# Performance work log

Hardware: AMD Instinct MI355X
Metric: run time of the kernel (lower is better)

## Reference

```python
import jax, jax.numpy as jnp
import numpy as np

D = 256        # n_unit
H = 2          # n_head
FF = 256       # n_hid
WIN = 99       # N-1 in source: row i attends to cols [i-99, i]
NEG = -1e30    # additive mask value (-inf in torch)
LN_EPS = 1e-5


def _layer_norm(x, w, b):
    mu = jnp.mean(x, axis=-1, keepdims=True)
    var = jnp.mean((x - mu) ** 2, axis=-1, keepdims=True)
    return (x - mu) * jax.lax.rsqrt(var + LN_EPS) * w + b


def _pos_encoding(S, d):
    pos = jnp.arange(S, dtype=jnp.float32)[:, None]                      # [S,1]
    div = jnp.exp(jnp.arange(0, d, 2, dtype=jnp.float32) * (-np.log(10000.0) / d))
    ang = pos * div                                                      # [S,d/2]
    return jnp.stack([jnp.sin(ang), jnp.cos(ang)], axis=-1).reshape(S, d)


def _band_mask(S):
    i = jnp.arange(S)[:, None]
    j = jnp.arange(S)[None, :]
    allowed = (j <= i) & (j >= i - WIN)
    return jnp.where(allowed, 0.0, NEG).astype(jnp.float32)             # [S,S]


def setup_inputs() -> dict:
    key = jax.random.key(0)
    ks = jax.random.split(key, 24)
    B, S, IN = 8, 2000, 256
    s = 0.02
    inp = {
        "src": jax.random.normal(ks[0], (B, S, IN), jnp.float32),
        "input_lengths": jax.random.randint(ks[1], (B,), 1, S + 1).astype(jnp.int64),
        # encoder Linear(in_size, n_unit); torch Linear weight is [out,in]
        "W_enc": jax.random.normal(ks[2], (D, IN), jnp.float32) * s,
        "b_enc": jnp.zeros((D,), jnp.float32),
        # MHA packed qkv projection
        "in_proj_w": jax.random.normal(ks[3], (3 * D, D), jnp.float32) * s,
        "in_proj_b": jnp.zeros((3 * D,), jnp.float32),
        "out_proj_w": jax.random.normal(ks[4], (D, D), jnp.float32) * s,
        "out_proj_b": jnp.zeros((D,), jnp.float32),
        "ln1_w": jnp.ones((D,), jnp.float32),
        "ln1_b": jnp.zeros((D,), jnp.float32),
        # FFN
        "lin1_w": jax.random.normal(ks[5], (FF, D), jnp.float32) * s,
        "lin1_b": jnp.zeros((FF,), jnp.float32),
        "lin2_w": jax.random.normal(ks[6], (D, FF), jnp.float32) * s,
        "lin2_b": jnp.zeros((D,), jnp.float32),
        "ln2_w": jnp.ones((D,), jnp.float32),
        "ln2_b": jnp.zeros((D,), jnp.float32),
        # output head
        "fc1_w": jax.random.normal(ks[7], (D // 4, D), jnp.float32) * s,
        "fc1_b": jnp.zeros((D // 4,), jnp.float32),
        "fc2_w": jax.random.normal(ks[8], (1, D // 4), jnp.float32) * s,
        "fc2_b": jnp.zeros((1,), jnp.float32),
    }
    return inp


def reference(src, input_lengths, W_enc, b_enc, in_proj_w, in_proj_b,
              out_proj_w, out_proj_b, ln1_w, ln1_b, lin1_w, lin1_b,
              lin2_w, lin2_b, ln2_w, ln2_b, fc1_w, fc1_b, fc2_w, fc2_b):
    B, S, _ = src.shape
    hd = D // H
    # input projection + positional encoding (dropout is identity at eval)
    x = src @ W_enc.T + b_enc                                            # [B,S,D]
    x = x + _pos_encoding(S, D)[None]
    # --- TransformerEncoderLayer (post-norm, relu) with banded causal mask ---
    qkv = x @ in_proj_w.T + in_proj_b                                    # [B,S,3D]
    q, k, v = jnp.split(qkv, 3, axis=-1)
    q = q.reshape(B, S, H, hd)
    k = k.reshape(B, S, H, hd)
    v = v.reshape(B, S, H, hd)
    scores = jnp.einsum('bihd,bjhd->bhij', q, k) / np.sqrt(hd)           # [B,H,S,S]
    scores = scores + _band_mask(S)[None, None]
    attn = jax.nn.softmax(scores, axis=-1)
    ctx = jnp.einsum('bhij,bjhd->bihd', attn, v).reshape(B, S, D)
    attn_out = ctx @ out_proj_w.T + out_proj_b
    x = _layer_norm(x + attn_out, ln1_w, ln1_b)
    ff = jax.nn.relu(x @ lin1_w.T + lin1_b) @ lin2_w.T + lin2_b
    x = _layer_norm(x + ff, ln2_w, ln2_b)
    # --- output head (no activation between fc1 and fc2, per source) ---
    out = x @ fc1_w.T + fc1_b                                            # [B,S,D/4]
    logits = out @ fc2_w.T + fc2_b                                       # [B,S,1]
    return logits.reshape(B, -1)                                         # [B,S]
```

## Files before the change

kernel.cpp:

```cpp
#include <hip/hip_runtime.h>
#include <math.h>

#define SLEN 2000
#define BATCH 8
#define MTOK 16000
#define WIN 99
#define XPAD 264

typedef __attribute__((ext_vector_type(8))) short short8;
typedef __attribute__((ext_vector_type(4))) float floatx4;

#define WAITVM0() __builtin_amdgcn_s_waitcnt(0x0F70)
#define WAITVM4() __builtin_amdgcn_s_waitcnt(0x0F74)

__device__ __forceinline__ float bf2f(unsigned int h) {
  union { unsigned int u; float f; } w; w.u = h << 16; return w.f;
}
__device__ __forceinline__ unsigned short f2bf(float f) {
  union { float f; unsigned int u; } w; w.f = f;
  return (unsigned short)((w.u + 0x7fffu + ((w.u >> 16) & 1u)) >> 16);
}

typedef const __attribute__((address_space(1))) unsigned int* gas_t;
typedef __attribute__((address_space(3))) unsigned int* las_t;
__device__ __forceinline__ void gload_lds16(const unsigned short* g, unsigned short* l) {
  __builtin_amdgcn_global_load_lds((gas_t)g, (las_t)l, 16, 0, 0);
}

__device__ __forceinline__ void cvt4(const float* __restrict__ in,
                                     unsigned short* __restrict__ out, int i) {
  float4 v = ((const float4*)in)[i];
  ushort4 o;
  o.x = f2bf(v.x); o.y = f2bf(v.y); o.z = f2bf(v.z); o.w = f2bf(v.w);
  ((ushort4*)out)[i] = o;
}

__global__ __launch_bounds__(256) void k_prep(
    const float* __restrict__ wenc,     unsigned short* __restrict__ wencb,
    const float* __restrict__ wqk,      unsigned short* __restrict__ wqkb,
    const float* __restrict__ wout,     unsigned short* __restrict__ woutb,
    const float* __restrict__ wl1,      unsigned short* __restrict__ wl1b,
    const float* __restrict__ wl2,      unsigned short* __restrict__ wl2b,
    float* __restrict__ pe,
    const float* __restrict__ fc1w, const float* __restrict__ fc1b,
    const float* __restrict__ fc2w, const float* __restrict__ fc2b,
    const float* __restrict__ ln2w, const float* __restrict__ ln2b,
    float* __restrict__ hp) {
  __shared__ float red0[4], red1[4];
  const int bx = blockIdx.x, tid = threadIdx.x;
  if (bx < 64)         { cvt4(wenc, wencb, bx * 256 + tid); }
  else if (bx < 256)   { cvt4(wqk,  wqkb,  (bx - 64) * 256 + tid); }
  else if (bx < 320)   { cvt4(wout, woutb, (bx - 256) * 256 + tid); }
  else if (bx < 384)   { cvt4(wl1,  wl1b,  (bx - 320) * 256 + tid); }
  else if (bx < 448)   { cvt4(wl2,  wl2b,  (bx - 384) * 256 + tid); }
  else if (bx < 948) {
    int i4 = (bx - 448) * 256 + tid;
    int e0 = i4 * 4;
    int s  = e0 >> 8;
    int d0 = e0 & 255;
    float dv0 = expf((float)(d0 >> 1) * -0.07195578415606394f);
    float dv1 = expf((float)((d0 >> 1) + 1) * -0.07195578415606394f);
    float a0 = (float)s * dv0, a1 = (float)s * dv1;
    ((float4*)pe)[i4] = make_float4(sinf(a0), cosf(a0), sinf(a1), cosf(a1));
  } else {
    int k = tid;
    float we = 0.f;
#pragma unroll 8
    for (int o = 0; o < 64; ++o) we += fc2w[o] * fc1w[o * 256 + k];
    float c1 = ln2w[k] * we;
    hp[k] = c1;
    float p0 = ln2b[k] * we;
    if (k < 64) p0 += fc2w[k] * fc1b[k];
    float s0 = p0, s1 = c1;
#pragma unroll
    for (int off = 32; off; off >>= 1) {
      s0 += __shfl_xor(s0, off);
      s1 += __shfl_xor(s1, off);
    }
    int wv = k >> 6;
    if ((k & 63) == 0) { red0[wv] = s0; red1[wv] = s1; }
    __syncthreads();
    if (k == 0) {
      hp[256] = red0[0] + red0[1] + red0[2] + red0[3] + fc2b[0];
      hp[257] = red1[0] + red1[1] + red1[2] + red1[3];
    }
  }
}

__global__ __launch_bounds__(256) void k_pre(
    const float* __restrict__ src,
    const unsigned short* __restrict__ wenc, const float* __restrict__ benc,
    const float* __restrict__ pe,
    const unsigned short* __restrict__ wqk, const float* __restrict__ bqk,
    unsigned short* __restrict__ xb, unsigned short* __restrict__ qkvb) {
  __shared__ __align__(16) unsigned short Xt[64 * XPAD];
  __shared__ __align__(16) unsigned short Bst[4][2][2048];
  const int tid = threadIdx.x, lane = tid & 63, w = tid >> 6;
  const int m0 = blockIdx.x * 64;
  const int kq = lane >> 4, ml = lane & 15;
  const int wcolg = w * 64;

  int grow[4], gsc[4];
#pragma unroll
  for (int i = 0; i < 4; ++i) {
    grow[i] = i * 16 + (lane >> 2);
    gsc[i]  = (lane & 3) ^ ((grow[i] >> 1) & 3);
  }

  auto issueB = [&](const unsigned short* W, int kt, int buf) {
#pragma unroll
    for (int i = 0; i < 4; ++i)
      gload_lds16(W + (size_t)(wcolg + grow[i]) * 256 + kt + gsc[i] * 8,
                  &Bst[w][buf][i * 512]);
  };
  auto readB = [&](int buf, int nt) -> short8 {
    int n = nt * 16 + ml;
    int sb = kq ^ ((n >> 1) & 3);
    return *(const short8*)&Bst[w][buf][n * 32 + sb * 8];
  };

  floatx4 acc[4][4] = {};
#pragma unroll
  for (int k8 = 0; k8 < 8; ++k8) {
    const int kt = k8 * 32;
    issueB(wenc, kt, k8 & 1);
    short8 af[4];
#pragma unroll
    for (int mt = 0; mt < 4; ++mt) {
      const float* ap = src + (size_t)(m0 + mt * 16 + ml) * 256 + kt + kq * 8;
      float4 v0 = *(const float4*)ap;
      float4 v1 = *(const float4*)(ap + 4);
      unsigned short t8[8] = {f2bf(v0.x), f2bf(v0.y), f2bf(v0.z), f2bf(v0.w),
                              f2bf(v1.x), f2bf(v1.y), f2bf(v1.z), f2bf(v1.w)};
      af[mt] = *(const short8*)t8;
    }
    WAITVM0();
#pragma unroll
    for (int nt = 0; nt < 4; ++nt) {
      short8 bf = readB(k8 & 1, nt);
#pragma unroll
      for (int mt = 0; mt < 4; ++mt)
        acc[mt][nt] = __builtin_amdgcn_mfma_f32_16x16x32_bf16(af[mt], bf, acc[mt][nt], 0, 0, 0);
    }
  }
#pragma unroll
  for (int mt = 0; mt < 4; ++mt)
#pragma unroll
    for (int nt = 0; nt < 4; ++nt)
#pragma unroll
      for (int r = 0; r < 4; ++r) {
        int lrow = mt * 16 + kq * 4 + r;
        int col  = wcolg + nt * 16 + ml;
        float v = acc[mt][nt][r] + benc[col]
                + pe[(size_t)((m0 + lrow) % SLEN) * 256 + col];
        unsigned short hv = f2bf(v);
        Xt[lrow * XPAD + col] = hv;
        xb[(size_t)(m0 + lrow) * 256 + col] = hv;
      }
  __syncthreads();

  for (int p = 0; p < 3; ++p) {
    const unsigned short* Wp = wqk + (size_t)p * 65536;
    floatx4 a2[4][4] = {};
    issueB(Wp, 0, 0);
#pragma unroll
    for (int k8 = 0; k8 < 7; ++k8) {
      issueB(Wp, (k8 + 1) * 32, (k8 + 1) & 1);
      WAITVM4();
      short8 af[4];
#pragma unroll
      for (int mt = 0; mt < 4; ++mt)
        af[mt] = *(const short8*)&Xt[(mt * 16 + ml) * XPAD + k8 * 32 + kq * 8];
#pragma unroll
      for (int nt = 0; nt < 4; ++nt) {
        short8 bf = readB(k8 & 1, nt);
#pragma unroll
        for (int mt = 0; mt < 4; ++mt)
          a2[mt][nt] = __builtin_amdgcn_mfma_f32_16x16x32_bf16(af[mt], bf, a2[mt][nt], 0, 0, 0);
      }
    }
    WAITVM0();
    {
      short8 af[4];
#pragma unroll
      for (int mt = 0; mt < 4; ++mt)
        af[mt] = *(const short8*)&Xt[(mt * 16 + ml) * XPAD + 224 + kq * 8];
#pragma unroll
      for (int nt = 0; nt < 4; ++nt) {
        short8 bf = readB(1, nt);
#pragma unroll
        for (int mt = 0; mt < 4; ++mt)
          a2[mt][nt] = __builtin_amdgcn_mfma_f32_16x16x32_bf16(af[mt], bf, a2[mt][nt], 0, 0, 0);
      }
    }
#pragma unroll
    for (int mt = 0; mt < 4; ++mt)
#pragma unroll
      for (int nt = 0; nt < 4; ++nt)
#pragma unroll
        for (int r = 0; r < 4; ++r) {
          int row = m0 + mt * 16 + kq * 4 + r;
          int cg  = p * 256 + wcolg + nt * 16 + ml;
          qkvb[(size_t)row * 768 + cg] = f2bf(a2[mt][nt][r] + bqk[cg]);
        }
  }
}

#define KPAD 136
#define VPAD 184
#define PPAD 132
#define UNION 176

__global__ __launch_bounds__(256) void k_attn_mfma(const unsigned short* __restrict__ qkv,
                                                   unsigned short* __restrict__ ctx) {
  __shared__ __align__(16) unsigned short KV[UNION * KPAD];
  __shared__ __align__(16) unsigned short Ps[4][16 * PPAD];
  const int tid  = threadIdx.x;
  const int lane = tid & 63;
  const int w    = tid >> 6;
  const int i0   = blockIdx.x * 64;
  const int b    = blockIdx.y;
  const int h    = blockIdx.z;
  const int jmin_u = i0 - WIN;
  const float scale = 0.08838834764831845f;

  const int qrow = i0 + w * 16 + (lane & 15);
  const unsigned short* qptr =
      qkv + (size_t)(b * SLEN + min(qrow, SLEN - 1)) * 768 + h * 128 + (lane >> 4) * 8;
  short8 qf[4];
#pragma unroll
  for (int kc = 0; kc < 4; ++kc) qf[kc] = *(const short8*)(qptr + kc * 32);

  for (int it = 0; it < 11; ++it) {
    int idx = it * 256 + tid;
    int row = idx >> 4;
    int c8  = idx & 15;
    int j = jmin_u + row;
    uint4 v = make_uint4(0u, 0u, 0u, 0u);
    if (j >= 0 && j < SLEN)
      v = *(const uint4*)(qkv + (size_t)(b * SLEN + j) * 768 + 256 + h * 128 + c8 * 8);
    *(uint4*)&KV[row * KPAD + c8 * 8] = v;
  }
  __syncthreads();

  const int koff = w * 16;
  floatx4 sc[8] = {};
#pragma unroll
  for (int kt = 0; kt < 8; ++kt) {
#pragma unroll
    for (int kc = 0; kc < 4; ++kc) {
      short8 kf = *(const short8*)&KV[(koff + kt * 16 + (lane & 15)) * KPAD
                                      + kc * 32 + (lane >> 4) * 8];
      sc[kt] = __builtin_amdgcn_mfma_f32_16x16x32_bf16(qf[kc], kf, sc[kt], 0, 0, 0);
    }
  }

  const int qme = i0 + w * 16 + (lane >> 4) * 4;
  const int jme = jmin_u + koff + (lane & 15);
  float mx[4] = {-1e30f, -1e30f, -1e30f, -1e30f};
#pragma unroll
  for (int kt = 0; kt < 8; ++kt) {
#pragma unroll
    for (int r = 0; r < 4; ++r) {
      int j = jme + kt * 16, q = qme + r;
      bool ok = (j >= 0) && (j >= q - WIN) && (j <= q);
      float s = ok ? sc[kt][r] : -1e30f;
      sc[kt][r] = s;
      mx[r] = fmaxf(mx[r], s);
    }
  }
#pragma unroll
  for (int r = 0; r < 4; ++r)
#pragma unroll
    for (int off = 8; off; off >>= 1) mx[r] = fmaxf(mx[r], __shfl_xor(mx[r], off, 16));

  float sum[4] = {0.f, 0.f, 0.f, 0.f};
#pragma unroll
  for (int kt = 0; kt < 8; ++kt)
#pragma unroll
    for (int r = 0; r < 4; ++r) {
      float e = __expf((sc[kt][r] - mx[r]) * scale);
      sc[kt][r] = e;
      sum[r] += e;
    }
#pragma unroll
  for (int r = 0; r < 4; ++r)
#pragma unroll
    for (int off = 8; off; off >>= 1) sum[r] += __shfl_xor(sum[r], off, 16);
  float rinv[4];
#pragma unroll
  for (int r = 0; r < 4; ++r) rinv[r] = 1.f / sum[r];

  unsigned short* pw = &Ps[w][0];
#pragma unroll
  for (int kt = 0; kt < 8; ++kt)
#pragma unroll
    for (int r = 0; r < 4; ++r)
      pw[((lane >> 4) * 4 + r) * PPAD + kt * 16 + (lane & 15)] = f2bf(sc[kt][r]);
  __syncthreads();

  for (int it = 0; it < 12; ++it) {
    int idx = it * 256 + tid;
    int grp = idx >> 6;
    int key = (grp >> 4) * 64 + (idx & 63);
    int c8  = grp & 15;
    if (key < UNION) {
      int j = jmin_u + key;
      uint4 v = make_uint4(0u, 0u, 0u, 0u);
      if (j >= 0 && j < SLEN)
        v = *(const uint4*)(qkv + (size_t)(b * SLEN + j) * 768 + 512 + h * 128 + c8 * 8);
      unsigned short e[8];
      *(uint4*)e = v;
      int d0 = c8 * 8;
#pragma unroll
      for (int i = 0; i < 8; ++i) KV[(d0 + i) * VPAD + key] = e[i];
    }
  }
  __syncthreads();

  floatx4 ov[8] = {};
#pragma unroll
  for (int kc = 0; kc < 4; ++kc) {
    short8 pf = *(const short8*)&pw[(lane & 15) * PPAD + kc * 32 + (lane >> 4) * 8];
#pragma unroll
    for (int dt = 0; dt < 8; ++dt) {
      short8 vf = *(const short8*)&KV[(dt * 16 + (lane & 15)) * VPAD
                                      + koff + kc * 32 + (lane >> 4) * 8];
      ov[dt] = __builtin_amdgcn_mfma_f32_16x16x32_bf16(pf, vf, ov[dt], 0, 0, 0);
    }
  }

#pragma unroll
  for (int dt = 0; dt < 8; ++dt)
#pragma unroll
    for (int r = 0; r < 4; ++r) {
      int q = qme + r;
      if (q < SLEN)
        ctx[(size_t)(b * SLEN + q) * 256 + h * 128 + dt * 16 + (lane & 15)] =
            f2bf(ov[dt][r] * rinv[r]);
    }
}

__global__ __launch_bounds__(256) void k_post(
    const unsigned short* __restrict__ ctx,
    const unsigned short* __restrict__ wout, const float* __restrict__ bout,
    const unsigned short* __restrict__ xb,
    const float* __restrict__ ln1w, const float* __restrict__ ln1b,
    const unsigned short* __restrict__ w1, const float* __restrict__ b1,
    const unsigned short* __restrict__ w2, const float* __restrict__ b2,
    const float* __restrict__ hp, float* __restrict__ out) {
  __shared__ __align__(16) unsigned short X1[64 * XPAD];
  __shared__ __align__(16) unsigned short Bst[4][2][2048];
  __shared__ float lnred[4][64][3];
  __shared__ float lnstat[64][2];
  __shared__ float lnp[512];
  __shared__ float c1s[256];
  const int tid = threadIdx.x, lane = tid & 63, w = tid >> 6;
  const int m0 = blockIdx.x * 64;
  const int kq = lane >> 4, ml = lane & 15;
  const int wcolg = w * 64;

  lnp[tid] = ln1w[tid];
  lnp[256 + tid] = ln1b[tid];
  c1s[tid] = hp[tid];
  const float c0h = hp[256], sc1 = hp[257];

  int grow[4], gsc[4];
#pragma unroll
  for (int i = 0; i < 4; ++i) {
    grow[i] = i * 16 + (lane >> 2);
    gsc[i]  = (lane & 3) ^ ((grow[i] >> 1) & 3);
  }
  auto issueB = [&](const unsigned short* W, int kt, int buf) {
#pragma unroll
    for (int i = 0; i < 4; ++i)
      gload_lds16(W + (size_t)(wcolg + grow[i]) * 256 + kt + gsc[i] * 8,
                  &Bst[w][buf][i * 512]);
  };
  auto readB = [&](int buf, int nt) -> short8 {
    int n = nt * 16 + ml;
    int sb = kq ^ ((n >> 1) & 3);
    return *(const short8*)&Bst[w][buf][n * 32 + sb * 8];
  };

  floatx4 acc[4][4] = {};
#pragma unroll
  for (int k8 = 0; k8 < 8; ++k8) {
    const int kt = k8 * 32;
    issueB(wout, kt, k8 & 1);
    short8 af[4];
#pragma unroll
    for (int mt = 0; mt < 4; ++mt)
      af[mt] = *(const short8*)(ctx + (size_t)(m0 + mt * 16 + ml) * 256 + kt + kq * 8);
    WAITVM0();
#pragma unroll
    for (int nt = 0; nt < 4; ++nt) {
      short8 bf = readB(k8 & 1, nt);
#pragma unroll
      for (int mt = 0; mt < 4; ++mt)
        acc[mt][nt] = __builtin_amdgcn_mfma_f32_16x16x32_bf16(af[mt], bf, acc[mt][nt], 0, 0, 0);
    }
  }
  float s_[4][4], q_[4][4];
#pragma unroll
  for (int mt = 0; mt < 4; ++mt)
#pragma unroll
    for (int r = 0; r < 4; ++r) { s_[mt][r] = 0.f; q_[mt][r] = 0.f; }
#pragma unroll
  for (int mt = 0; mt < 4; ++mt)
#pragma unroll
    for (int nt = 0; nt < 4; ++nt)
#pragma unroll
      for (int r = 0; r < 4; ++r) {
        int lrow = mt * 16 + kq * 4 + r;
        int col  = wcolg + nt * 16 + ml;
        float v = acc[mt][nt][r] + bout[col]
                + bf2f(xb[(size_t)(m0 + lrow) * 256 + col]);
        acc[mt][nt][r] = v;
        s_[mt][r] += v;
        q_[mt][r] += v * v;
      }
#pragma unroll
  for (int mt = 0; mt < 4; ++mt)
#pragma unroll
    for (int r = 0; r < 4; ++r) {
#pragma unroll
      for (int off = 8; off; off >>= 1) {
        s_[mt][r] += __shfl_xor(s_[mt][r], off, 16);
        q_[mt][r] += __shfl_xor(q_[mt][r], off, 16);
      }
      if (ml == 0) {
        int lrow = mt * 16 + kq * 4 + r;
        lnred[w][lrow][0] = s_[mt][r];
        lnred[w][lrow][1] = q_[mt][r];
      }
    }
  __syncthreads();
  if (tid < 64) {
    float s = lnred[0][tid][0] + lnred[1][tid][0] + lnred[2][tid][0] + lnred[3][tid][0];
    float q = lnred[0][tid][1] + lnred[1][tid][1] + lnred[2][tid][1] + lnred[3][tid][1];
    float mu  = s * (1.f / 256.f);
    float var = q * (1.f / 256.f) - mu * mu;
    lnstat[tid][0] = mu;
    lnstat[tid][1] = rsqrtf(var + 1e-5f);
  }
  __syncthreads();
  floatx4 x1sav[4][4];
#pragma unroll
  for (int mt = 0; mt < 4; ++mt)
#pragma unroll
    for (int r = 0; r < 4; ++r) {
      int lrow = mt * 16 + kq * 4 + r;
      float mu = lnstat[lrow][0], rr = lnstat[lrow][1];
#pragma unroll
      for (int nt = 0; nt < 4; ++nt) {
        int col = wcolg + nt * 16 + ml;
        float x1 = (acc[mt][nt][r] - mu) * rr * lnp[col] + lnp[256 + col];
        x1sav[mt][nt][r] = x1;
        X1[lrow * XPAD + col] = f2bf(x1);
      }
    }
  __syncthreads();

#pragma unroll
  for (int mt = 0; mt < 4; ++mt)
#pragma unroll
    for (int nt = 0; nt < 4; ++nt) acc[mt][nt] = (floatx4){0.f, 0.f, 0.f, 0.f};
  issueB(w1, 0, 0);
#pragma unroll
  for (int k8 = 0; k8 < 7; ++k8) {
    issueB(w1, (k8 + 1) * 32, (k8 + 1) & 1);
    WAITVM4();
    short8 af[4];
#pragma unroll
    for (int mt = 0; mt < 4; ++mt)
      af[mt] = *(const short8*)&X1[(mt * 16 + ml) * XPAD + k8 * 32 + kq * 8];
#pragma unroll
    for (int nt = 0; nt < 4; ++nt) {
      short8 bf = readB(k8 & 1, nt);
#pragma unroll
      for (int mt = 0; mt < 4; ++mt)
        acc[mt][nt] = __builtin_amdgcn_mfma_f32_16x16x32_bf16(af[mt], bf, acc[mt][nt], 0, 0, 0);
    }
  }
  WAITVM0();
  {
    short8 af[4];
#pragma unroll
    for (int mt = 0; mt < 4; ++mt)
      af[mt] = *(const short8*)&X1[(mt * 16 + ml) * XPAD + 224 + kq * 8];
#pragma unroll
    for (int nt = 0; nt < 4; ++nt) {
      short8 bf = readB(1, nt);
#pragma unroll
      for (int mt = 0; mt < 4; ++mt)
        acc[mt][nt] = __builtin_amdgcn_mfma_f32_16x16x32_bf16(af[mt], bf, acc[mt][nt], 0, 0, 0);
    }
  }
  __syncthreads();
#pragma unroll
  for (int mt = 0; mt < 4; ++mt)
#pragma unroll
    for (int nt = 0; nt < 4; ++nt)
#pragma unroll
      for (int r = 0; r < 4; ++r) {
        int lrow = mt * 16 + kq * 4 + r;
        int col  = wcolg + nt * 16 + ml;
        X1[lrow * XPAD + col] = f2bf(fmaxf(acc[mt][nt][r] + b1[col], 0.f));
      }
  __syncthreads();

#pragma unroll
  for (int mt = 0; mt < 4; ++mt)
#pragma unroll
    for (int nt = 0; nt < 4; ++nt) acc[mt][nt] = (floatx4){0.f, 0.f, 0.f, 0.f};
  issueB(w2, 0, 0);
#pragma unroll
  for (int k8 = 0; k8 < 7; ++k8) {
    issueB(w2, (k8 + 1) * 32, (k8 + 1) & 1);
    WAITVM4();
    short8 af[4];
#pragma unroll
    for (int mt = 0; mt < 4; ++mt)
      af[mt] = *(const short8*)&X1[(mt * 16 + ml) * XPAD + k8 * 32 + kq * 8];
#pragma unroll
    for (int nt = 0; nt < 4; ++nt) {
      short8 bf = readB(k8 & 1, nt);
#pragma unroll
      for (int mt = 0; mt < 4; ++mt)
        acc[mt][nt] = __builtin_amdgcn_mfma_f32_16x16x32_bf16(af[mt], bf, acc[mt][nt], 0, 0, 0);
    }
  }
  WAITVM0();
  {
    short8 af[4];
#pragma unroll
    for (int mt = 0; mt < 4; ++mt)
      af[mt] = *(const short8*)&X1[(mt * 16 + ml) * XPAD + 224 + kq * 8];
#pragma unroll
    for (int nt = 0; nt < 4; ++nt) {
      short8 bf = readB(1, nt);
#pragma unroll
      for (int mt = 0; mt < 4; ++mt)
        acc[mt][nt] = __builtin_amdgcn_mfma_f32_16x16x32_bf16(af[mt], bf, acc[mt][nt], 0, 0, 0);
    }
  }
  float ss[4][4], qq[4][4], dd[4][4];
#pragma unroll
  for (int mt = 0; mt < 4; ++mt)
#pragma unroll
    for (int r = 0; r < 4; ++r) { ss[mt][r] = 0.f; qq[mt][r] = 0.f; dd[mt][r] = 0.f; }
#pragma unroll
  for (int mt = 0; mt < 4; ++mt)
#pragma unroll
    for (int nt = 0; nt < 4; ++nt)
#pragma unroll
      for (int r = 0; r < 4; ++r) {
        int col = wcolg + nt * 16 + ml;
        float v = acc[mt][nt][r] + b2[col] + x1sav[mt][nt][r];
        ss[mt][r] += v;
        qq[mt][r] += v * v;
        dd[mt][r] += v * c1s[col];
      }
#pragma unroll
  for (int mt = 0; mt < 4; ++mt)
#pragma unroll
    for (int r = 0; r < 4; ++r) {
#pragma unroll
      for (int off = 8; off; off >>= 1) {
        ss[mt][r] += __shfl_xor(ss[mt][r], off, 16);
        qq[mt][r] += __shfl_xor(qq[mt][r], off, 16);
        dd[mt][r] += __shfl_xor(dd[mt][r], off, 16);
      }
      if (ml == 0) {
        int lrow = mt * 16 + kq * 4 + r;
        lnred[w][lrow][0] = ss[mt][r];
        lnred[w][lrow][1] = qq[mt][r];
        lnred[w][lrow][2] = dd[mt][r];
      }
    }
  __syncthreads();
  if (tid < 64) {
    float s = lnred[0][tid][0] + lnred[1][tid][0] + lnred[2][tid][0] + lnred[3][tid][0];
    float q = lnred[0][tid][1] + lnred[1][tid][1] + lnred[2][tid][1] + lnred[3][tid][1];
    float d = lnred[0][tid][2] + lnred[1][tid][2] + lnred[2][tid][2] + lnred[3][tid][2];
    float mu  = s * (1.f / 256.f);
    float var = q * (1.f / 256.f) - mu * mu;
    float rr  = rsqrtf(var + 1e-5f);
    out[m0 + tid] = rr * (d - mu * sc1) + c0h;
  }
}

extern "C" void kernel_launch(void* const* d_in, const int* in_sizes, int n_in,
                              void* d_out, int out_size, void* d_ws, size_t ws_size,
                              hipStream_t stream) {
  const float* src        = (const float*)d_in[0];
  const float* W_enc      = (const float*)d_in[2];
  const float* b_enc      = (const float*)d_in[3];
  const float* in_proj_w  = (const float*)d_in[4];
  const float* in_proj_b  = (const float*)d_in[5];
  const float* out_proj_w = (const float*)d_in[6];
  const float* out_proj_b = (const float*)d_in[7];
  const float* ln1_w      = (const float*)d_in[8];
  const float* ln1_b      = (const float*)d_in[9];
  const float* lin1_w     = (const float*)d_in[10];
  const float* lin1_b     = (const float*)d_in[11];
  const float* lin2_w     = (const float*)d_in[12];
  const float* lin2_b     = (const float*)d_in[13];
  const float* ln2_w      = (const float*)d_in[14];
  const float* ln2_b      = (const float*)d_in[15];
  const float* fc1_w      = (const float*)d_in[16];
  const float* fc1_b      = (const float*)d_in[17];
  const float* fc2_w      = (const float*)d_in[18];
  const float* fc2_b      = (const float*)d_in[19];

  char* p = (char*)d_ws;
  float* pe            = (float*)p;           p += (size_t)SLEN * 256 * 4;
  float* hp            = (float*)p;           p += 2048;
  unsigned short* xb   = (unsigned short*)p;  p += (size_t)MTOK * 256 * 2;
  unsigned short* qkvb = (unsigned short*)p;  p += (size_t)MTOK * 768 * 2;
  unsigned short* ctxb = (unsigned short*)p;  p += (size_t)MTOK * 256 * 2;
  unsigned short* wencb= (unsigned short*)p;  p += 256 * 256 * 2;
  unsigned short* wqkb = (unsigned short*)p;  p += 768 * 256 * 2;
  unsigned short* woutb= (unsigned short*)p;  p += 256 * 256 * 2;
  unsigned short* wl1b = (unsigned short*)p;  p += 256 * 256 * 2;
  unsigned short* wl2b = (unsigned short*)p;  p += 256 * 256 * 2;

  k_prep<<<949, 256, 0, stream>>>(W_enc, wencb, in_proj_w, wqkb,
                                  out_proj_w, woutb, lin1_w, wl1b, lin2_w, wl2b,
                                  pe, fc1_w, fc1_b, fc2_w, fc2_b, ln2_w, ln2_b, hp);
  k_pre<<<MTOK / 64, 256, 0, stream>>>(src, wencb, b_enc, pe, wqkb, in_proj_b, xb, qkvb);
  k_attn_mfma<<<dim3((SLEN + 63) / 64, BATCH, 2), 256, 0, stream>>>(qkvb, ctxb);
  k_post<<<MTOK / 64, 256, 0, stream>>>(ctxb, woutb, out_proj_b, xb, ln1_w, ln1_b,
                                        wl1b, lin1_b, wl2b, lin2_b, hp, (float*)d_out);
}
```

Before: 173.5 us.

## Use 8 waves per block in projection kernels and read weights directly from global

k_pre and k_post now launch with 512 threads (8 waves), each wave owning a narrower column slice (32 columns, or 96 for the QKV projection). The LDS-staged, double-buffered weight loads via global_load_lds are removed, and B fragments are read straight from global memory, which should mostly hit in cache. This aims to raise occupancy and latency hiding and to shrink LDS use. In exchange it loses the explicit prefetch pipelining and issues more redundant global weight reads.

```diff
diff --git a/kernel.cpp b/kernel.cpp
--- a/kernel.cpp
+++ b/kernel.cpp
@@ -10,21 +10,12 @@
 typedef __attribute__((ext_vector_type(8))) short short8;
 typedef __attribute__((ext_vector_type(4))) float floatx4;
 
-#define WAITVM0() __builtin_amdgcn_s_waitcnt(0x0F70)
-#define WAITVM4() __builtin_amdgcn_s_waitcnt(0x0F74)
-
 __device__ __forceinline__ float bf2f(unsigned int h) {
   union { unsigned int u; float f; } w; w.u = h << 16; return w.f;
 }
 __device__ __forceinline__ unsigned short f2bf(float f) {
   union { float f; unsigned int u; } w; w.f = f;
   return (unsigned short)((w.u + 0x7fffu + ((w.u >> 16) & 1u)) >> 16);
-}
-
-typedef const __attribute__((address_space(1))) unsigned int* gas_t;
-typedef __attribute__((address_space(3))) unsigned int* las_t;
-__device__ __forceinline__ void gload_lds16(const unsigned short* g, unsigned short* l) {
-  __builtin_amdgcn_global_load_lds((gas_t)g, (las_t)l, 16, 0, 0);
 }
 
 __device__ __forceinline__ void cvt4(const float* __restrict__ in,
@@ -87,121 +78,85 @@
   }
 }
 
-__global__ __launch_bounds__(256) void k_pre(
+__global__ __launch_bounds__(512) void k_pre(
     const float* __restrict__ src,
     const unsigned short* __restrict__ wenc, const float* __restrict__ benc,
     const float* __restrict__ pe,
     const unsigned short* __restrict__ wqk, const float* __restrict__ bqk,
     unsigned short* __restrict__ xb, unsigned short* __restrict__ qkvb) {
   __shared__ __align__(16) unsigned short Xt[64 * XPAD];
-  __shared__ __align__(16) unsigned short Bst[4][2][2048];
   const int tid = threadIdx.x, lane = tid & 63, w = tid >> 6;
   const int m0 = blockIdx.x * 64;
   const int kq = lane >> 4, ml = lane & 15;
-  const int wcolg = w * 64;
-
-  int grow[4], gsc[4];
-#pragma unroll
-  for (int i = 0; i < 4; ++i) {
-    grow[i] = i * 16 + (lane >> 2);
-    gsc[i]  = (lane & 3) ^ ((grow[i] >> 1) & 3);
-  }
-
-  auto issueB = [&](const unsigned short* W, int kt, int buf) {
-#pragma unroll
-    for (int i = 0; i < 4; ++i)
-      gload_lds16(W + (size_t)(wcolg + grow[i]) * 256 + kt + gsc[i] * 8,
-                  &Bst[w][buf][i * 512]);
-  };
-  auto readB = [&](int buf, int nt) -> short8 {
-    int n = nt * 16 + ml;
-    int sb = kq ^ ((n >> 1) & 3);
-    return *(const short8*)&Bst[w][buf][n * 32 + sb * 8];
-  };
-
-  floatx4 acc[4][4] = {};
-#pragma unroll
-  for (int k8 = 0; k8 < 8; ++k8) {
-    const int kt = k8 * 32;
-    issueB(wenc, kt, k8 & 1);
-    short8 af[4];
-#pragma unroll
-    for (int mt = 0; mt < 4; ++mt) {
-      const float* ap = src + (size_t)(m0 + mt * 16 + ml) * 256 + kt + kq * 8;
-      float4 v0 = *(const float4*)ap;
-      float4 v1 = *(const float4*)(ap + 4);
-      unsigned short t8[8] = {f2bf(v0.x), f2bf(v0.y), f2bf(v0.z), f2bf(v0.w),
-                              f2bf(v1.x), f2bf(v1.y), f2bf(v1.z), f2bf(v1.w)};
-      af[mt] = *(const short8*)t8;
-    }
-    WAITVM0();
-#pragma unroll
-    for (int nt = 0; nt < 4; ++nt) {
-      short8 bf = readB(k8 & 1, nt);
+
+  {
+    const int cb = w * 32;
+    floatx4 acc[4][2] = {};
+#pragma unroll
+    for (int k8 = 0; k8 < 8; ++k8) {
+      const int kt = k8 * 32;
+      short8 af[4];
+#pragma unroll
+      for (int mt = 0; mt < 4; ++mt) {
+        const float* ap = src + (size_t)(m0 + mt * 16 + ml) * 256 + kt + kq * 8;
+        float4 v0 = *(const float4*)ap;
+        float4 v1 = *(const float4*)(ap + 4);
+        unsigned short t8[8] = {f2bf(v0.x), f2bf(v0.y), f2bf(v0.z), f2bf(v0.w),
+                                f2bf(v1.x), f2bf(v1.y), f2bf(v1.z), f2bf(v1.w)};
+        af[mt] = *(const short8*)t8;
+      }
+#pragma unroll
+      for (int nt = 0; nt < 2; ++nt) {
+        short8 bf = *(const short8*)(wenc + (size_t)(cb + nt * 16 + ml) * 256 + kt + kq * 8);
+#pragma unroll
+        for (int mt = 0; mt < 4; ++mt)
+          acc[mt][nt] = __builtin_amdgcn_mfma_f32_16x16x32_bf16(af[mt], bf, acc[mt][nt], 0, 0, 0);
+      }
+    }
+#pragma unroll
+    for (int mt = 0; mt < 4; ++mt)
+#pragma unroll
+      for (int nt = 0; nt < 2; ++nt)
+#pragma unroll
+        for (int r = 0; r < 4; ++r) {
+          int lrow = mt * 16 + kq * 4 + r;
+          int col  = cb + nt * 16 + ml;
+          float v = acc[mt][nt][r] + benc[col]
+                  + pe[(size_t)((m0 + lrow) % SLEN) * 256 + col];
+          unsigned short hv = f2bf(v);
+          Xt[lrow * XPAD + col] = hv;
+          xb[(size_t)(m0 + lrow) * 256 + col] = hv;
+        }
+  }
+  __syncthreads();
+
+  {
+    const int cb = w * 96;
+    floatx4 acc[4][6] = {};
+#pragma unroll
+    for (int k8 = 0; k8 < 8; ++k8) {
+      const int kt = k8 * 32;
+      short8 af[4];
 #pragma unroll
       for (int mt = 0; mt < 4; ++mt)
-        acc[mt][nt] = __builtin_amdgcn_mfma_f32_16x16x32_bf16(af[mt], bf, acc[mt][nt], 0, 0, 0);
-    }
-  }
-#pragma unroll
-  for (int mt = 0; mt < 4; ++mt)
-#pragma unroll
-    for (int nt = 0; nt < 4; ++nt)
-#pragma unroll
-      for (int r = 0; r < 4; ++r) {
-        int lrow = mt * 16 + kq * 4 + r;
-        int col  = wcolg + nt * 16 + ml;
-        float v = acc[mt][nt][r] + benc[col]
-                + pe[(size_t)((m0 + lrow) % SLEN) * 256 + col];
-        unsigned short hv = f2bf(v);
-        Xt[lrow * XPAD + col] = hv;
-        xb[(size_t)(m0 + lrow) * 256 + col] = hv;
-      }
-  __syncthreads();
-
-  for (int p = 0; p < 3; ++p) {
-    const unsigned short* Wp = wqk + (size_t)p * 65536;
-    floatx4 a2[4][4] = {};
-    issueB(Wp, 0, 0);
-#pragma unroll
-    for (int k8 = 0; k8 < 7; ++k8) {
-      issueB(Wp, (k8 + 1) * 32, (k8 + 1) & 1);
-      WAITVM4();
-      short8 af[4];
-#pragma unroll
-      for (int mt = 0; mt < 4; ++mt)
-        af[mt] = *(const short8*)&Xt[(mt * 16 + ml) * XPAD + k8 * 32 + kq * 8];
-#pragma unroll
-      for (int nt = 0; nt < 4; ++nt) {
-        short8 bf = readB(k8 & 1, nt);
+        af[mt] = *(const short8*)&Xt[(mt * 16 + ml) * XPAD + kt + kq * 8];
+#pragma unroll
+      for (int nt = 0; nt < 6; ++nt) {
+        short8 bf = *(const short8*)(wqk + (size_t)(cb + nt * 16 + ml) * 256 + kt + kq * 8);
 #pragma unroll
         for (int mt = 0; mt < 4; ++mt)
-          a2[mt][nt] = __builtin_amdgcn_mfma_f32_16x16x32_bf16(af[mt], bf, a2[mt][nt], 0, 0, 0);
-      }
-    }
-    WAITVM0();
-    {
-      short8 af[4];
-#pragma unroll
-      for (int mt = 0; mt < 4; ++mt)
-        af[mt] = *(const short8*)&Xt[(mt * 16 + ml) * XPAD + 224 + kq * 8];
-#pragma unroll
-      for (int nt = 0; nt < 4; ++nt) {
-        short8 bf = readB(1, nt);
-#pragma unroll
-        for (int mt = 0; mt < 4; ++mt)
-          a2[mt][nt] = __builtin_amdgcn_mfma_f32_16x16x32_bf16(af[mt], bf, a2[mt][nt], 0, 0, 0);
+          acc[mt][nt] = __builtin_amdgcn_mfma_f32_16x16x32_bf16(af[mt], bf, acc[mt][nt], 0, 0, 0);
       }
     }
 #pragma unroll
     for (int mt = 0; mt < 4; ++mt)
 #pragma unroll
-      for (int nt = 0; nt < 4; ++nt)
+      for (int nt = 0; nt < 6; ++nt)
 #pragma unroll
         for (int r = 0; r < 4; ++r) {
           int row = m0 + mt * 16 + kq * 4 + r;
-          int cg  = p * 256 + wcolg + nt * 16 + ml;
-          qkvb[(size_t)row * 768 + cg] = f2bf(a2[mt][nt][r] + bqk[cg]);
+          int cg  = cb + nt * 16 + ml;
+          qkvb[(size_t)row * 768 + cg] = f2bf(acc[mt][nt][r] + bqk[cg]);
         }
   }
 }
@@ -341,7 +296,7 @@
     }
 }
 
-__global__ __launch_bounds__(256) void k_post(
+__global__ __launch_bounds__(512) void k_post(
     const unsigned short* __restrict__ ctx,
     const unsigned short* __restrict__ wout, const float* __restrict__ bout,
     const unsigned short* __restrict__ xb,
@@ -350,52 +305,33 @@
     const unsigned short* __restrict__ w2, const float* __restrict__ b2,
     const float* __restrict__ hp, float* __restrict__ out) {
   __shared__ __align__(16) unsigned short X1[64 * XPAD];
-  __shared__ __align__(16) unsigned short Bst[4][2][2048];
-  __shared__ float lnred[4][64][3];
+  __shared__ float lnred[8][64][3];
   __shared__ float lnstat[64][2];
   __shared__ float lnp[512];
   __shared__ float c1s[256];
   const int tid = threadIdx.x, lane = tid & 63, w = tid >> 6;
   const int m0 = blockIdx.x * 64;
   const int kq = lane >> 4, ml = lane & 15;
-  const int wcolg = w * 64;
-
-  lnp[tid] = ln1w[tid];
-  lnp[256 + tid] = ln1b[tid];
-  c1s[tid] = hp[tid];
+  const int cb = w * 32;
+
+  if (tid < 256) {
+    lnp[tid] = ln1w[tid];
+    lnp[256 + tid] = ln1b[tid];
+    c1s[tid] = hp[tid];
+  }
   const float c0h = hp[256], sc1 = hp[257];
 
-  int grow[4], gsc[4];
-#pragma unroll
-  for (int i = 0; i < 4; ++i) {
-    grow[i] = i * 16 + (lane >> 2);
-    gsc[i]  = (lane & 3) ^ ((grow[i] >> 1) & 3);
-  }
-  auto issueB = [&](const unsigned short* W, int kt, int buf) {
-#pragma unroll
-    for (int i = 0; i < 4; ++i)
-      gload_lds16(W + (size_t)(wcolg + grow[i]) * 256 + kt + gsc[i] * 8,
-                  &Bst[w][buf][i * 512]);
-  };
-  auto readB = [&](int buf, int nt) -> short8 {
-    int n = nt * 16 + ml;
-    int sb = kq ^ ((n >> 1) & 3);
-    return *(const short8*)&Bst[w][buf][n * 32 + sb * 8];
-  };
-
-  floatx4 acc[4][4] = {};
+  floatx4 acc[4][2] = {};
 #pragma unroll
   for (int k8 = 0; k8 < 8; ++k8) {
     const int kt = k8 * 32;
-    issueB(wout, kt, k8 & 1);
     short8 af[4];
 #pragma unroll
     for (int mt = 0; mt < 4; ++mt)
       af[mt] = *(const short8*)(ctx + (size_t)(m0 + mt * 16 + ml) * 256 + kt + kq * 8);
-    WAITVM0();
-#pragma unroll
-    for (int nt = 0; nt < 4; ++nt) {
-      short8 bf = readB(k8 & 1, nt);
+#pragma unroll
+    for (int nt = 0; nt < 2; ++nt) {
+      short8 bf = *(const short8*)(wout + (size_t)(cb + nt * 16 + ml) * 256 + kt + kq * 8);
 #pragma unroll
       for (int mt = 0; mt < 4; ++mt)
         acc[mt][nt] = __builtin_amdgcn_mfma_f32_16x16x32_bf16(af[mt], bf, acc[mt][nt], 0, 0, 0);
@@ -409,11 +345,11 @@
 #pragma unroll
   for (int mt = 0; mt < 4; ++mt)
 #pragma unroll
-    for (int nt = 0; nt < 4; ++nt)
+    for (int nt = 0; nt < 2; ++nt)
 #pragma unroll
       for (int r = 0; r < 4; ++r) {
         int lrow = mt * 16 + kq * 4 + r;
-        int col  = wcolg + nt * 16 + ml;
+        int col  = cb + nt * 16 + ml;
         float v = acc[mt][nt][r] + bout[col]
                 + bf2f(xb[(size_t)(m0 + lrow) * 256 + col]);
         acc[mt][nt][r] = v;
@@ -437,15 +373,16 @@
     }
   __syncthreads();
   if (tid < 64) {
-    float s = lnred[0][tid][0] + lnred[1][tid][0] + lnred[2][tid][0] + lnred[3][tid][0];
-    float q = lnred[0][tid][1] + lnred[1][tid][1] + lnred[2][tid][1] + lnred[3][tid][1];
+    float s = 0.f, q = 0.f;
+#pragma unroll
+    for (int i = 0; i < 8; ++i) { s += lnred[i][tid][0]; q += lnred[i][tid][1]; }
     float mu  = s * (1.f / 256.f);
     float var = q * (1.f / 256.f) - mu * mu;
     lnstat[tid][0] = mu;
     lnstat[tid][1] = rsqrtf(var + 1e-5f);
   }
   __syncthreads();
-  floatx4 x1sav[4][4];
+  floatx4 x1sav[4][2];
 #pragma unroll
   for (int mt = 0; mt < 4; ++mt)
 #pragma unroll
@@ -453,8 +390,8 @@
       int lrow = mt * 16 + kq * 4 + r;
       float mu = lnstat[lrow][0], rr = lnstat[lrow][1];
 #pragma unroll
-      for (int nt = 0; nt < 4; ++nt) {
-        int col = wcolg + nt * 16 + ml;
+      for (int nt = 0; nt < 2; ++nt) {
+        int col = cb + nt * 16 + ml;
         float x1 = (acc[mt][nt][r] - mu) * rr * lnp[col] + lnp[256 + col];
         x1sav[mt][nt][r] = x1;
         X1[lrow * XPAD + col] = f2bf(x1);
@@ -465,98 +402,66 @@
 #pragma unroll
   for (int mt = 0; mt < 4; ++mt)
 #pragma unroll
-    for (int nt = 0; nt < 4; ++nt) acc[mt][nt] = (floatx4){0.f, 0.f, 0.f, 0.f};
-  issueB(w1, 0, 0);
-#pragma unroll
-  for (int k8 = 0; k8 < 7; ++k8) {
-    issueB(w1, (k8 + 1) * 32, (k8 + 1) & 1);
-    WAITVM4();
+    for (int nt = 0; nt < 2; ++nt) acc[mt][nt] = (floatx4){0.f, 0.f, 0.f, 0.f};
+#pragma unroll
+  for (int k8 = 0; k8 < 8; ++k8) {
+    const int kt = k8 * 32;
     short8 af[4];
 #pragma unroll
     for (int mt = 0; mt < 4; ++mt)
-      af[mt] = *(const short8*)&X1[(mt * 16 + ml) * XPAD + k8 * 32 + kq * 8];
-#pragma unroll
-    for (int nt = 0; nt < 4; ++nt) {
-      short8 bf = readB(k8 & 1, nt);
+      af[mt] = *(const short8*)&X1[(mt * 16 + ml) * XPAD + kt + kq * 8];
+#pragma unroll
+    for (int nt = 0; nt < 2; ++nt) {
+      short8 bf = *(const short8*)(w1 + (size_t)(cb + nt * 16 + ml) * 256 + kt + kq * 8);
 #pragma unroll
       for (int mt = 0; mt < 4; ++mt)
         acc[mt][nt] = __builtin_amdgcn_mfma_f32_16x16x32_bf16(af[mt], bf, acc[mt][nt], 0, 0, 0);
     }
   }
-  WAITVM0();
-  {
+  __syncthreads();
+#pragma unroll
+  for (int mt = 0; mt < 4; ++mt)
+#pragma unroll
+    for (int nt = 0; nt < 2; ++nt)
+#pragma unroll
+      for (int r = 0; r < 4; ++r) {
+        int lrow = mt * 16 + kq * 4 + r;
+        int col  = cb + nt * 16 + ml;
+        X1[lrow * XPAD + col] = f2bf(fmaxf(acc[mt][nt][r] + b1[col], 0.f));
+      }
+  __syncthreads();
+
+#pragma unroll
+  for (int mt = 0; mt < 4; ++mt)
+#pragma unroll
+    for (int nt = 0; nt < 2; ++nt) acc[mt][nt] = (floatx4){0.f, 0.f, 0.f, 0.f};
+#pragma unroll
+  for (int k8 = 0; k8 < 8; ++k8) {
+    const int kt = k8 * 32;
     short8 af[4];
 #pragma unroll
     for (int mt = 0; mt < 4; ++mt)
-      af[mt] = *(const short8*)&X1[(mt * 16 + ml) * XPAD + 224 + kq * 8];
-#pragma unroll
-    for (int nt = 0; nt < 4; ++nt) {
-      short8 bf = readB(1, nt);
+      af[mt] = *(const short8*)&X1[(mt * 16 + ml) * XPAD + kt + kq * 8];
+#pragma unroll
+    for (int nt = 0; nt < 2; ++nt) {
+      short8 bf = *(const short8*)(w2 + (size_t)(cb + nt * 16 + ml) * 256 + kt + kq * 8);
 #pragma unroll
       for (int mt = 0; mt < 4; ++mt)
         acc[mt][nt] = __builtin_amdgcn_mfma_f32_16x16x32_bf16(af[mt], bf, acc[mt][nt], 0, 0, 0);
     }
   }
-  __syncthreads();
-#pragma unroll
-  for (int mt = 0; mt < 4; ++mt)
-#pragma unroll
-    for (int nt = 0; nt < 4; ++nt)
+  float ss[4][4], qq[4][4], dd[4][4];
+#pragma unroll
+  for (int mt = 0; mt < 4; ++mt)
+#pragma unroll
+    for (int r = 0; r < 4; ++r) { ss[mt][r] = 0.f; qq[mt][r] = 0.f; dd[mt][r] = 0.f; }
+#pragma unroll
+  for (int mt = 0; mt < 4; ++mt)
+#pragma unroll
+    for (int nt = 0; nt < 2; ++nt)
 #pragma unroll
       for (int r = 0; r < 4; ++r) {
-        int lrow = mt * 16 + kq * 4 + r;
-        int col  = wcolg + nt * 16 + ml;
-        X1[lrow * XPAD + col] = f2bf(fmaxf(acc[mt][nt][r] + b1[col], 0.f));
-      }
-  __syncthreads();
-
-#pragma unroll
-  for (int mt = 0; mt < 4; ++mt)
-#pragma unroll
-    for (int nt = 0; nt < 4; ++nt) acc[mt][nt] = (floatx4){0.f, 0.f, 0.f, 0.f};
-  issueB(w2, 0, 0);
-#pragma unroll
-  for (int k8 = 0; k8 < 7; ++k8) {
-    issueB(w2, (k8 + 1) * 32, (k8 + 1) & 1);
-    WAITVM4();
-    short8 af[4];
-#pragma unroll
-    for (int mt = 0; mt < 4; ++mt)
-      af[mt] = *(const short8*)&X1[(mt * 16 + ml) * XPAD + k8 * 32 + kq * 8];
-#pragma unroll
-    for (int nt = 0; nt < 4; ++nt) {
-      short8 bf = readB(k8 & 1, nt);
-#pragma unroll
-      for (int mt = 0; mt < 4; ++mt)
-        acc[mt][nt] = __builtin_amdgcn_mfma_f32_16x16x32_bf16(af[mt], bf, acc[mt][nt], 0, 0, 0);
-    }
-  }
-  WAITVM0();
-  {
-    short8 af[4];
-#pragma unroll
-    for (int mt = 0; mt < 4; ++mt)
-      af[mt] = *(const short8*)&X1[(mt * 16 + ml) * XPAD + 224 + kq * 8];
-#pragma unroll
-    for (int nt = 0; nt < 4; ++nt) {
-      short8 bf = readB(1, nt);
-#pragma unroll
-      for (int mt = 0; mt < 4; ++mt)
-        acc[mt][nt] = __builtin_amdgcn_mfma_f32_16x16x32_bf16(af[mt], bf, acc[mt][nt], 0, 0, 0);
-    }
-  }
-  float ss[4][4], qq[4][4], dd[4][4];
-#pragma unroll
-  for (int mt = 0; mt < 4; ++mt)
-#pragma unroll
-    for (int r = 0; r < 4; ++r) { ss[mt][r] = 0.f; qq[mt][r] = 0.f; dd[mt][r] = 0.f; }
-#pragma unroll
-  for (int mt = 0; mt < 4; ++mt)
-#pragma unroll
-    for (int nt = 0; nt < 4; ++nt)
-#pragma unroll
-      for (int r = 0; r < 4; ++r) {
-        int col = wcolg + nt * 16 + ml;
+        int col = cb + nt * 16 + ml;
         float v = acc[mt][nt][r] + b2[col] + x1sav[mt][nt][r];
         ss[mt][r] += v;
         qq[mt][r] += v * v;
@@ -581,9 +486,13 @@
     }
   __syncthreads();
   if (tid < 64) {
-    float s = lnred[0][tid][0] + lnred[1][tid][0] + lnred[2][tid][0] + lnred[3][tid][0];
-    float q = lnred[0][tid][1] + lnred[1][tid][1] + lnred[2][tid][1] + lnred[3][tid][1];
-    float d = lnred[0][tid][2] + lnred[1][tid][2] + lnred[2][tid][2] + lnred[3][tid][2];
+    float s = 0.f, q = 0.f, d = 0.f;
+#pragma unroll
+    for (int i = 0; i < 8; ++i) {
+      s += lnred[i][tid][0];
+      q += lnred[i][tid][1];
+      d += lnred[i][tid][2];
+    }
     float mu  = s * (1.f / 256.f);
     float var = q * (1.f / 256.f) - mu * mu;
     float rr  = rsqrtf(var + 1e-5f);
@@ -629,8 +538,8 @@
   k_prep<<<949, 256, 0, stream>>>(W_enc, wencb, in_proj_w, wqkb,
                                   out_proj_w, woutb, lin1_w, wl1b, lin2_w, wl2b,
                                   pe, fc1_w, fc1_b, fc2_w, fc2_b, ln2_w, ln2_b, hp);
-  k_pre<<<MTOK / 64, 256, 0, stream>>>(src, wencb, b_enc, pe, wqkb, in_proj_b, xb, qkvb);
+  k_pre<<<MTOK / 64, 512, 0, stream>>>(src, wencb, b_enc, pe, wqkb, in_proj_b, xb, qkvb);
   k_attn_mfma<<<dim3((SLEN + 63) / 64, BATCH, 2), 256, 0, stream>>>(qkvb, ctxb);
-  k_post<<<MTOK / 64, 256, 0, stream>>>(ctxb, woutb, out_proj_b, xb, ln1_w, ln1_b,
+  k_post<<<MTOK / 64, 512, 0, stream>>>(ctxb, woutb, out_proj_b, xb, ln1_w, ln1_b,
                                         wl1b, lin1_b, wl2b, lin2_b, hp, (float*)d_out);
 }
```

New measurement: 188.8 us. 8.8% more time.
